# Kernel tuning notes

Measured on AMD Instinct MI355X. Metric: run time of the kernel, lower is better.

## Reference

```python
import jax, jax.numpy as jnp
import numpy as np

H = 16
D_MODEL = 1024
D_K = D_MODEL // H
NEG = -1e9


def setup_inputs() -> dict:
    key = jax.random.key(0)
    ks = jax.random.split(key, 12)
    B, S, D = 2, 2048, D_MODEL
    scale = 1.0 / np.sqrt(D)
    inp = {
        "query": jax.random.normal(ks[0], (B, S, D), jnp.float32),
        "key": jax.random.normal(ks[1], (B, S, D), jnp.float32),
        "value": jax.random.normal(ks[2], (B, S, D), jnp.float32),
        "mask": jax.random.randint(ks[3], (B, S, S), 0, 2, jnp.int32),
        # four Linear(d_model, d_model) layers: q, k, v, out projections
        "Wq": jax.random.normal(ks[4], (D, D), jnp.float32) * scale,
        "bq": jnp.zeros((D,), jnp.float32),
        "Wk": jax.random.normal(ks[5], (D, D), jnp.float32) * scale,
        "bk": jnp.zeros((D,), jnp.float32),
        "Wv": jax.random.normal(ks[6], (D, D), jnp.float32) * scale,
        "bv": jnp.zeros((D,), jnp.float32),
        "Wo": jax.random.normal(ks[7], (D, D), jnp.float32) * scale,
        "bo": jnp.zeros((D,), jnp.float32),
    }
    return inp


def reference(query, key, value, mask, Wq, bq, Wk, bk, Wv, bv, Wo, bo):
    B, S, D = query.shape
    # QKV projections, then split into heads: [B, H, S, D_K]
    def proj(x, W, b):
        return (x @ W + b).reshape(B, S, H, D_K).transpose(0, 2, 1, 3)

    q = proj(query, Wq, bq)
    k = proj(key, Wk, bk)
    v = proj(value, Wv, bv)

    # scaled dot-product attention; scale by sqrt(d_k) (query.size(-1) after split)
    scores = jnp.einsum("bhqd,bhkd->bhqk", q, k) / np.sqrt(D_K)
    scores = jnp.where(mask[:, None, :, :] == 0, NEG, scores)
    p = jax.nn.softmax(scores, axis=-1)  # dropout is identity in eval mode
    x = jnp.einsum("bhqk,bhkd->bhqd", p, v)

    # merge heads and apply output projection
    x = x.transpose(0, 2, 1, 3).reshape(B, S, H * D_K)
    return x @ Wo + bo
```

## Files before the change

### kernel.cpp

```cpp
#include <hip/hip_runtime.h>

typedef _Float16 f16;
typedef __attribute__((ext_vector_type(2))) _Float16 f16x2;
typedef __attribute__((ext_vector_type(4))) _Float16 f16x4;
typedef __attribute__((ext_vector_type(8))) _Float16 f16x8;
typedef __attribute__((ext_vector_type(4))) float f32x4;

#define MFMA16(A_, B_, C_) __builtin_amdgcn_mfma_f32_16x16x32_f16(A_, B_, C_, 0, 0, 0)
#define EXP2(x) __builtin_amdgcn_exp2f(x)

#define NHEAD 16
#define SEQ 2048
#define DM 1024
#define DK 64
#define NBATCH 2
#define M_TOT (NBATCH * SEQ)

#define GLDS(gp, lp)                                                                     \
    __builtin_amdgcn_global_load_lds((const __attribute__((address_space(1))) void*)(gp), \
                                     (__attribute__((address_space(3))) void*)(lp), 16, 0, 0)

__global__ void pack_mask_k(const int* __restrict__ mask, unsigned long long* __restrict__ mp, int nwords) {
    int lane = threadIdx.x & 63;
    int gw = (blockIdx.x * blockDim.x + threadIdx.x) >> 6;
    int nw = (gridDim.x * blockDim.x) >> 6;
    for (int w = gw; w < nwords; w += nw) {
        int v = mask[(size_t)w * 64 + lane];
        unsigned long long bits = __ballot(v != 0);
        if (lane == 0) mp[w] = bits;
    }
}

__global__ __launch_bounds__(256) void cvt_x_k(const float* __restrict__ xq, const float* __restrict__ xk,
                                               const float* __restrict__ xv, f16* __restrict__ oq,
                                               f16* __restrict__ ok, f16* __restrict__ ov) {
    const float* src = blockIdx.z == 0 ? xq : (blockIdx.z == 1 ? xk : xv);
    f16* dst = blockIdx.z == 0 ? oq : (blockIdx.z == 1 ? ok : ov);
    size_t i = ((size_t)blockIdx.x * 256 + threadIdx.x) * 8;
    float4 a = *(const float4*)&src[i];
    float4 b = *(const float4*)&src[i + 4];
    f16x8 h;
    h[0] = (f16)a.x; h[1] = (f16)a.y; h[2] = (f16)a.z; h[3] = (f16)a.w;
    h[4] = (f16)b.x; h[5] = (f16)b.y; h[6] = (f16)b.z; h[7] = (f16)b.w;
    *(f16x8*)&dst[i] = h;
}

__global__ __launch_bounds__(256) void wt_k(const float* __restrict__ Wq, const float* __restrict__ Wk,
                                            const float* __restrict__ Wv, const float* __restrict__ Wo,
                                            f16* __restrict__ Wt) {
    __shared__ float T[64][65];
    const int z = blockIdx.z;
    const float* W = z == 0 ? Wq : (z == 1 ? Wk : (z == 2 ? Wv : Wo));
    f16* out = Wt + (size_t)z * DM * DM;
    const int k0 = blockIdx.y * 64, n0 = blockIdx.x * 64;
    const int r = threadIdx.x >> 2, q = threadIdx.x & 3;
    const float4* s = (const float4*)&W[(size_t)(k0 + r) * DM + n0 + q * 16];
    float4 v0 = s[0], v1 = s[1], v2 = s[2], v3 = s[3];
    T[r][q * 16 + 0] = v0.x; T[r][q * 16 + 1] = v0.y; T[r][q * 16 + 2] = v0.z; T[r][q * 16 + 3] = v0.w;
    T[r][q * 16 + 4] = v1.x; T[r][q * 16 + 5] = v1.y; T[r][q * 16 + 6] = v1.z; T[r][q * 16 + 7] = v1.w;
    T[r][q * 16 + 8] = v2.x; T[r][q * 16 + 9] = v2.y; T[r][q * 16 + 10] = v2.z; T[r][q * 16 + 11] = v2.w;
    T[r][q * 16 + 12] = v3.x; T[r][q * 16 + 13] = v3.y; T[r][q * 16 + 14] = v3.z; T[r][q * 16 + 15] = v3.w;
    __syncthreads();
    f16x8 h0, h1;
#pragma unroll
    for (int j = 0; j < 8; ++j) {
        h0[j] = (f16)T[q * 16 + j][r];
        h1[j] = (f16)T[q * 16 + 8 + j][r];
    }
    *(f16x8*)&out[(size_t)(n0 + r) * DM + k0 + q * 16] = h0;
    *(f16x8*)&out[(size_t)(n0 + r) * DM + k0 + q * 16 + 8] = h1;
}

__global__ __launch_bounds__(256) void vt_k(const f16* __restrict__ Vh, f16* __restrict__ VhT) {
    __shared__ f16 T[64][72];
    const int bh = blockIdx.y;
    const int s0 = blockIdx.x * 64;
    const f16* src = Vh + (size_t)bh * SEQ * DK;
    f16* dst = VhT + (size_t)bh * DK * SEQ;
    const int r = threadIdx.x >> 2, q = threadIdx.x & 3;
    f16x8 a = *(const f16x8*)&src[(size_t)(s0 + r) * DK + q * 16];
    f16x8 b = *(const f16x8*)&src[(size_t)(s0 + r) * DK + q * 16 + 8];
    *(f16x8*)&T[r][q * 16] = a;
    *(f16x8*)&T[r][q * 16 + 8] = b;
    __syncthreads();
    f16x8 o0, o1;
#pragma unroll
    for (int j = 0; j < 8; ++j) {
        o0[j] = T[q * 16 + j][r];
        o1[j] = T[q * 16 + 8 + j][r];
    }
    *(f16x8*)&dst[(size_t)r * SEQ + s0 + q * 16] = o0;
    *(f16x8*)&dst[(size_t)r * SEQ + s0 + q * 16 + 8] = o1;
}

__device__ __forceinline__ void gemm_core(const f16* __restrict__ A, const f16* __restrict__ Bt,
                                          int m0, int n0, f16* Al, f16* Bl, f32x4 acc[4][4], int tid) {
    const int lane = tid & 63;
    const int wv = tid >> 6;
    const int wr = wv >> 1, wc = wv & 1;
    const int g = lane >> 4, c = lane & 15;

    for (int k0 = 0; k0 < DM; k0 += 64) {
#pragma unroll
        for (int j = 0; j < 4; ++j) {
            int chunk = j * 256 + tid;
            int row = chunk >> 3, cc = chunk & 7;
            int ccs = cc ^ (row & 7);
            GLDS(&A[(size_t)(m0 + row) * DM + k0 + ccs * 8], &Al[chunk * 8]);
        }
#pragma unroll
        for (int j = 0; j < 4; ++j) {
            int chunk = j * 256 + tid;
            int row = chunk >> 3, cc = chunk & 7;
            int ccs = cc ^ (row & 7);
            GLDS(&Bt[(size_t)(n0 + row) * DM + k0 + ccs * 8], &Bl[chunk * 8]);
        }
        __syncthreads();
#pragma unroll
        for (int ks = 0; ks < 2; ++ks) {
            f16x8 af[4], bf[4];
#pragma unroll
            for (int mi = 0; mi < 4; ++mi) {
                int row = wr * 64 + mi * 16 + c;
                af[mi] = *(const f16x8*)&Al[row * 64 + ((ks * 4 + g) ^ (row & 7)) * 8];
            }
#pragma unroll
            for (int ni = 0; ni < 4; ++ni) {
                int row = wc * 64 + ni * 16 + c;
                bf[ni] = *(const f16x8*)&Bl[row * 64 + ((ks * 4 + g) ^ (row & 7)) * 8];
            }
#pragma unroll
            for (int mi = 0; mi < 4; ++mi)
#pragma unroll
                for (int ni = 0; ni < 4; ++ni)
                    acc[mi][ni] = MFMA16(af[mi], bf[ni], acc[mi][ni]);
        }
        __syncthreads();
    }
}

__global__ __launch_bounds__(256) void gemm_qkv2_k(
    const f16* __restrict__ Xq, const f16* __restrict__ Xk, const f16* __restrict__ Xv,
    const f16* __restrict__ Wt, const float* __restrict__ bq, const float* __restrict__ bk,
    const float* __restrict__ bv, f16* __restrict__ Qh, f16* __restrict__ Kh, f16* __restrict__ Vh) {
    __shared__ f16 Al[128 * 64];
    __shared__ f16 Bl[128 * 64];
    const int which = blockIdx.z;
    const f16* A = which == 0 ? Xq : (which == 1 ? Xk : Xv);
    const f16* Bt = Wt + (size_t)which * DM * DM;
    const float* bias = which == 0 ? bq : (which == 1 ? bk : bv);
    f16* OUT = which == 0 ? Qh : (which == 1 ? Kh : Vh);

    const int tid = threadIdx.x, lane = tid & 63, wv = tid >> 6;
    const int wr = wv >> 1, wc = wv & 1, g = lane >> 4, c = lane & 15;
    const int m0 = blockIdx.y * 128, n0 = blockIdx.x * 128;

    f32x4 acc[4][4] = {};
    gemm_core(A, Bt, m0, n0, Al, Bl, acc, tid);

#pragma unroll
    for (int ni = 0; ni < 4; ++ni) {
        int n = n0 + wc * 64 + ni * 16 + c;
        float bias_n = bias[n];
        int hh = n >> 6, d = n & 63;
#pragma unroll
        for (int mi = 0; mi < 4; ++mi) {
            int mbase = m0 + wr * 64 + mi * 16 + g * 4;
#pragma unroll
            for (int r = 0; r < 4; ++r) {
                int m = mbase + r;
                int bb = m >> 11, s = m & (SEQ - 1);
                OUT[(((size_t)(bb * NHEAD + hh)) * SEQ + s) * DK + d] = (f16)(acc[mi][ni][r] + bias_n);
            }
        }
    }
}

__global__ __launch_bounds__(256) void gemm_out2_k(
    const f16* __restrict__ Xo, const f16* __restrict__ Wto, const float* __restrict__ bo,
    float* __restrict__ OUT) {
    __shared__ f16 Al[128 * 64];
    __shared__ f16 Bl[128 * 64];
    const int tid = threadIdx.x, lane = tid & 63, wv = tid >> 6;
    const int wr = wv >> 1, wc = wv & 1, g = lane >> 4, c = lane & 15;
    const int m0 = blockIdx.y * 128, n0 = blockIdx.x * 128;

    f32x4 acc[4][4] = {};
    gemm_core(Xo, Wto, m0, n0, Al, Bl, acc, tid);

#pragma unroll
    for (int ni = 0; ni < 4; ++ni) {
        int n = n0 + wc * 64 + ni * 16 + c;
        float bias_n = bo[n];
#pragma unroll
        for (int mi = 0; mi < 4; ++mi) {
            int mbase = m0 + wr * 64 + mi * 16 + g * 4;
#pragma unroll
            for (int r = 0; r < 4; ++r) {
                int m = mbase + r;
                OUT[(size_t)m * DM + n] = acc[mi][ni][r] + bias_n;
            }
        }
    }
}

#define QBLK 128
#define NHALF 2
#define KTH (SEQ / 64 / NHALF)
#define CSC 0.18033688011112042f

__global__ __launch_bounds__(512) void attn_k(
    const f16* __restrict__ Qh, const f16* __restrict__ Kh, const f16* __restrict__ VhT,
    const unsigned long long* __restrict__ mp, f16* __restrict__ O0, f16* __restrict__ O1,
    float2* __restrict__ ml) {
    __shared__ f16 Kl[2][4096];
    __shared__ f16 Vl[2][4096];
    __shared__ f16 Plds[8][16 * 72];

    const int tid = threadIdx.x, lane = tid & 63, wv = tid >> 6;
    const int g = lane >> 4, c = lane & 15;
    const int qt = blockIdx.x, hh = blockIdx.y;
    const int b = blockIdx.z >> 1, half = blockIdx.z & 1;
    const size_t headoff = ((size_t)(b * NHEAD + hh)) * SEQ * DK;
    const f16* Qb = Qh + headoff;
    const f16* Kb = Kh + headoff + (size_t)half * (SEQ / NHALF) * DK;
    const f16* VbT = VhT + headoff + (size_t)half * (SEQ / NHALF);

    const int srow = tid >> 3, scc = (tid & 7) ^ (srow & 7);

#define STAGE_ATTN(jj, pp)                                                      \
    do {                                                                        \
        GLDS(&Kb[(size_t)((jj)*64 + srow) * DK + scc * 8], &Kl[pp][tid * 8]);   \
        GLDS(&VbT[(size_t)srow * SEQ + (jj)*64 + scc * 8], &Vl[pp][tid * 8]);   \
    } while (0)

    const int qrow = qt * QBLK + wv * 16 + c;
    f16x8 bq0 = *(const f16x8*)&Qb[(size_t)qrow * DK + g * 8];
    f16x8 bq1 = *(const f16x8*)&Qb[(size_t)qrow * DK + 32 + g * 8];
    bq0 *= (f16)CSC;
    bq1 *= (f16)CSC;

    f32x4 acc[4] = {};
    float l_run = 0.f;

    const unsigned long long* mrow = mp + ((size_t)b * SEQ + qrow) * (SEQ / 64) + half * KTH;
    unsigned long long wq_cur = mrow[0];

    STAGE_ATTN(0, 0);
    int p = 0;
    for (int j = 0; j < KTH; ++j) {
        __syncthreads();
        if (j + 1 < KTH) STAGE_ATTN(j + 1, p ^ 1);
        unsigned long long wq_nxt = (j + 1 < KTH) ? mrow[j + 1] : 0ull;

        f32x4 sc[4];
        __builtin_amdgcn_s_setprio(1);
#pragma unroll
        for (int nk = 0; nk < 4; ++nk) {
            int row = nk * 16 + c;
            f16x8 k0 = *(const f16x8*)&Kl[p][row * 64 + ((g ^ (row & 7)) * 8)];
            f16x8 k1 = *(const f16x8*)&Kl[p][row * 64 + (((4 + g) ^ (row & 7)) * 8)];
            f32x4 z = {};
            z = MFMA16(k0, bq0, z);
            z = MFMA16(k1, bq1, z);
            sc[nk] = z;
        }
        __builtin_amdgcn_s_setprio(0);

        unsigned long long wq = wq_cur >> (g * 4);
        float ps = 0.f;
#pragma unroll
        for (int nk = 0; nk < 4; ++nk) {
            unsigned int nib = (unsigned int)(wq >> (nk * 16)) & 0xFu;
#pragma unroll
            for (int r = 0; r < 4; ++r) {
                float pp = EXP2(sc[nk][r]);
                pp = (nib & (1u << r)) ? pp : 0.f;
                sc[nk][r] = pp;
                ps += pp;
            }
        }
        ps += __shfl_xor(ps, 16);
        ps += __shfl_xor(ps, 32);
        l_run += ps;

#pragma unroll
        for (int nk = 0; nk < 4; ++nk)
#pragma unroll
            for (int r2 = 0; r2 < 2; ++r2) {
                f16x2 pw = {(f16)sc[nk][r2 * 2], (f16)sc[nk][r2 * 2 + 1]};
                *(f16x2*)&Plds[wv][c * 72 + nk * 16 + g * 4 + r2 * 2] = pw;
            }
        f16x8 pb0 = *(const f16x8*)&Plds[wv][c * 72 + g * 8];
        f16x8 pb1 = *(const f16x8*)&Plds[wv][c * 72 + 32 + g * 8];

        __builtin_amdgcn_s_setprio(1);
#pragma unroll
        for (int nd = 0; nd < 4; ++nd) {
            int row = nd * 16 + c;
            f16x8 v0 = *(const f16x8*)&Vl[p][row * 64 + ((g ^ (row & 7)) * 8)];
            f16x8 v1 = *(const f16x8*)&Vl[p][row * 64 + (((4 + g) ^ (row & 7)) * 8)];
            acc[nd] = MFMA16(v0, pb0, acc[nd]);
            acc[nd] = MFMA16(v1, pb1, acc[nd]);
        }
        __builtin_amdgcn_s_setprio(0);

        wq_cur = wq_nxt;
        p ^= 1;
    }

    f16* Opart = half ? O1 : O0;
    {
        float inv = l_run > 0.f ? 1.0f / l_run : 0.f;
        size_t hrow = headoff / DK + qrow;
#pragma unroll
        for (int nd = 0; nd < 4; ++nd) {
            f16x4 o;
#pragma unroll
            for (int r = 0; r < 4; ++r) o[r] = (f16)(acc[nd][r] * inv);
            *(f16x4*)&Opart[hrow * DK + nd * 16 + g * 4] = o;
        }
        if (g == 0) ml[(size_t)half * (M_TOT * NHEAD) + hrow] = make_float2(0.f, l_run);
    }
#undef STAGE_ATTN
}

__global__ __launch_bounds__(256) void combine_k(const f16* __restrict__ O0, const f16* __restrict__ O1,
                                                 const float2* __restrict__ ml, f16* __restrict__ Xo) {
    const int row = blockIdx.x * 32 + (threadIdx.x >> 3);
    const int d0 = (threadIdx.x & 7) * 8;
    const int b = row >> 15, hh = (row >> 11) & 15, q = row & (SEQ - 1);
    float2 a = ml[row];
    float2 bb = ml[(M_TOT * NHEAD) + row];
    float m = fmaxf(a.x, bb.x);
    float w0 = a.y * EXP2(a.x - m);
    float w1 = bb.y * EXP2(bb.x - m);
    float inv = 1.0f / (w0 + w1);
    float a0 = w0 * inv, a1 = w1 * inv;
    f16x8 o0 = *(const f16x8*)&O0[(size_t)row * DK + d0];
    f16x8 o1 = *(const f16x8*)&O1[(size_t)row * DK + d0];
    f16x8 o;
#pragma unroll
    for (int i = 0; i < 8; ++i) o[i] = (f16)(a0 * (float)o0[i] + a1 * (float)o1[i]);
    *(f16x8*)&Xo[((size_t)(b * SEQ + q)) * DM + hh * DK + d0] = o;
}

extern "C" void kernel_launch(void* const* d_in, const int* in_sizes, int n_in,
                              void* d_out, int out_size, void* d_ws, size_t ws_size,
                              hipStream_t stream) {
    const float* query = (const float*)d_in[0];
    const float* key_ = (const float*)d_in[1];
    const float* value = (const float*)d_in[2];
    const int* mask = (const int*)d_in[3];
    const float* Wq = (const float*)d_in[4];
    const float* bq = (const float*)d_in[5];
    const float* Wk = (const float*)d_in[6];
    const float* bk = (const float*)d_in[7];
    const float* Wv = (const float*)d_in[8];
    const float* bv = (const float*)d_in[9];
    const float* Wo = (const float*)d_in[10];
    const float* bo = (const float*)d_in[11];
    float* out = (float*)d_out;

    char* ws = (char*)d_ws;
    const size_t headsz = (size_t)NBATCH * NHEAD * SEQ * DK * sizeof(f16);
    unsigned long long* mp = (unsigned long long*)(ws);
    f16* Qh = (f16*)(ws + (1 << 20));
    f16* Kh = (f16*)(ws + (1 << 20) + headsz);
    f16* Vh = (f16*)(ws + (1 << 20) + 2 * headsz);
    f16* Xhq = (f16*)(ws + (1 << 20) + 3 * headsz);
    f16* Xhk = (f16*)(ws + (1 << 20) + 4 * headsz);
    f16* Xhv = (f16*)(ws + (1 << 20) + 5 * headsz);
    f16* Wt = (f16*)(ws + (1 << 20) + 6 * headsz);
    float2* ml = (float2*)(ws + (1 << 20) + 7 * headsz);
    f16* VhT = Xhq;
    f16* Xo = Xhq;

    int nwords = NBATCH * SEQ * (SEQ / 64);
    hipLaunchKernelGGL(pack_mask_k, dim3(512), dim3(256), 0, stream, mask, mp, nwords);
    hipLaunchKernelGGL(cvt_x_k, dim3(M_TOT * DM / (8 * 256), 1, 3), dim3(256), 0, stream,
                       query, key_, value, Xhq, Xhk, Xhv);
    hipLaunchKernelGGL(wt_k, dim3(DM / 64, DM / 64, 4), dim3(256), 0, stream, Wq, Wk, Wv, Wo, Wt);
    hipLaunchKernelGGL(gemm_qkv2_k, dim3(DM / 128, M_TOT / 128, 3), dim3(256), 0, stream,
                       Xhq, Xhk, Xhv, Wt, bq, bk, bv, Qh, Kh, Vh);
    hipLaunchKernelGGL(vt_k, dim3(SEQ / 64, NBATCH * NHEAD), dim3(256), 0, stream, Vh, VhT);
    hipLaunchKernelGGL(attn_k, dim3(SEQ / QBLK, NHEAD, NBATCH * NHALF), dim3(512), 0, stream,
                       Qh, Kh, VhT, mp, Xhk, Xhv, ml);
    hipLaunchKernelGGL(combine_k, dim3(M_TOT * NHEAD / 32), dim3(256), 0, stream, Xhk, Xhv, ml, Xo);
    hipLaunchKernelGGL(gemm_out2_k, dim3(DM / 128, M_TOT / 128), dim3(256), 0, stream,
                       Xo, Wt + (size_t)3 * DM * DM, bo, out);
}
```

Baseline: 179.4 us.

## Merge prep kernels, write V transposed from GEMM, fold softmax scale into Wq

Folds the mask packing, input conversion and weight transpose into one prep kernel, which removes two launches. The QKV GEMM epilogue now writes V straight into the transposed layout, so the separate transpose kernel goes away. The softmax scale is folded into Wq and bq at prep time, so the per-block Q multiply in attention is dropped. Also changed: the row-sum shuffle reduction moves out of the loop to run once at the end, and the P staging stride is padded to cut LDS bank conflicts. Risks are the transposed V stores, which are scattered 8-byte writes, and an extra fp16 rounding step on the scaled weights.

After: 170.6 us. 5.0% less time.

```diff
diff --git a/kernel.cpp b/kernel.cpp
--- a/kernel.cpp
+++ b/kernel.cpp
@@ -15,82 +15,65 @@
 #define DK 64
 #define NBATCH 2
 #define M_TOT (NBATCH * SEQ)
+#define CSC 0.18033688011112042f
 
 #define GLDS(gp, lp)                                                                     \
     __builtin_amdgcn_global_load_lds((const __attribute__((address_space(1))) void*)(gp), \
                                      (__attribute__((address_space(3))) void*)(lp), 16, 0, 0)
 
-__global__ void pack_mask_k(const int* __restrict__ mask, unsigned long long* __restrict__ mp, int nwords) {
-    int lane = threadIdx.x & 63;
-    int gw = (blockIdx.x * blockDim.x + threadIdx.x) >> 6;
-    int nw = (gridDim.x * blockDim.x) >> 6;
-    for (int w = gw; w < nwords; w += nw) {
-        int v = mask[(size_t)w * 64 + lane];
-        unsigned long long bits = __ballot(v != 0);
-        if (lane == 0) mp[w] = bits;
-    }
-}
-
-__global__ __launch_bounds__(256) void cvt_x_k(const float* __restrict__ xq, const float* __restrict__ xk,
-                                               const float* __restrict__ xv, f16* __restrict__ oq,
-                                               f16* __restrict__ ok, f16* __restrict__ ov) {
-    const float* src = blockIdx.z == 0 ? xq : (blockIdx.z == 1 ? xk : xv);
-    f16* dst = blockIdx.z == 0 ? oq : (blockIdx.z == 1 ? ok : ov);
-    size_t i = ((size_t)blockIdx.x * 256 + threadIdx.x) * 8;
-    float4 a = *(const float4*)&src[i];
-    float4 b = *(const float4*)&src[i + 4];
-    f16x8 h;
-    h[0] = (f16)a.x; h[1] = (f16)a.y; h[2] = (f16)a.z; h[3] = (f16)a.w;
-    h[4] = (f16)b.x; h[5] = (f16)b.y; h[6] = (f16)b.z; h[7] = (f16)b.w;
-    *(f16x8*)&dst[i] = h;
-}
-
-__global__ __launch_bounds__(256) void wt_k(const float* __restrict__ Wq, const float* __restrict__ Wk,
-                                            const float* __restrict__ Wv, const float* __restrict__ Wo,
-                                            f16* __restrict__ Wt) {
+__global__ __launch_bounds__(256) void prep_k(
+    const int* __restrict__ mask, unsigned long long* __restrict__ mp,
+    const float* __restrict__ xq, const float* __restrict__ xk, const float* __restrict__ xv,
+    f16* __restrict__ oq, f16* __restrict__ ok, f16* __restrict__ ov,
+    const float* __restrict__ Wq, const float* __restrict__ Wk,
+    const float* __restrict__ Wv, const float* __restrict__ Wo, f16* __restrict__ Wt) {
     __shared__ float T[64][65];
-    const int z = blockIdx.z;
-    const float* W = z == 0 ? Wq : (z == 1 ? Wk : (z == 2 ? Wv : Wo));
-    f16* out = Wt + (size_t)z * DM * DM;
-    const int k0 = blockIdx.y * 64, n0 = blockIdx.x * 64;
-    const int r = threadIdx.x >> 2, q = threadIdx.x & 3;
-    const float4* s = (const float4*)&W[(size_t)(k0 + r) * DM + n0 + q * 16];
-    float4 v0 = s[0], v1 = s[1], v2 = s[2], v3 = s[3];
-    T[r][q * 16 + 0] = v0.x; T[r][q * 16 + 1] = v0.y; T[r][q * 16 + 2] = v0.z; T[r][q * 16 + 3] = v0.w;
-    T[r][q * 16 + 4] = v1.x; T[r][q * 16 + 5] = v1.y; T[r][q * 16 + 6] = v1.z; T[r][q * 16 + 7] = v1.w;
-    T[r][q * 16 + 8] = v2.x; T[r][q * 16 + 9] = v2.y; T[r][q * 16 + 10] = v2.z; T[r][q * 16 + 11] = v2.w;
-    T[r][q * 16 + 12] = v3.x; T[r][q * 16 + 13] = v3.y; T[r][q * 16 + 14] = v3.z; T[r][q * 16 + 15] = v3.w;
-    __syncthreads();
-    f16x8 h0, h1;
-#pragma unroll
-    for (int j = 0; j < 8; ++j) {
-        h0[j] = (f16)T[q * 16 + j][r];
-        h1[j] = (f16)T[q * 16 + 8 + j][r];
-    }
-    *(f16x8*)&out[(size_t)(n0 + r) * DM + k0 + q * 16] = h0;
-    *(f16x8*)&out[(size_t)(n0 + r) * DM + k0 + q * 16 + 8] = h1;
-}
-
-__global__ __launch_bounds__(256) void vt_k(const f16* __restrict__ Vh, f16* __restrict__ VhT) {
-    __shared__ f16 T[64][72];
-    const int bh = blockIdx.y;
-    const int s0 = blockIdx.x * 64;
-    const f16* src = Vh + (size_t)bh * SEQ * DK;
-    f16* dst = VhT + (size_t)bh * DK * SEQ;
-    const int r = threadIdx.x >> 2, q = threadIdx.x & 3;
-    f16x8 a = *(const f16x8*)&src[(size_t)(s0 + r) * DK + q * 16];
-    f16x8 b = *(const f16x8*)&src[(size_t)(s0 + r) * DK + q * 16 + 8];
-    *(f16x8*)&T[r][q * 16] = a;
-    *(f16x8*)&T[r][q * 16 + 8] = b;
-    __syncthreads();
-    f16x8 o0, o1;
-#pragma unroll
-    for (int j = 0; j < 8; ++j) {
-        o0[j] = T[q * 16 + j][r];
-        o1[j] = T[q * 16 + 8 + j][r];
-    }
-    *(f16x8*)&dst[(size_t)r * SEQ + s0 + q * 16] = o0;
-    *(f16x8*)&dst[(size_t)r * SEQ + s0 + q * 16 + 8] = o1;
+    const int z = blockIdx.z, bx = blockIdx.x, tid = threadIdx.x;
+    if (z < 3) {
+        const float* src = z == 0 ? xq : (z == 1 ? xk : xv);
+        f16* dst = z == 0 ? oq : (z == 1 ? ok : ov);
+        size_t i = ((size_t)bx * 256 + tid) * 8;
+        float4 a = *(const float4*)&src[i];
+        float4 b = *(const float4*)&src[i + 4];
+        f16x8 h;
+        h[0] = (f16)a.x; h[1] = (f16)a.y; h[2] = (f16)a.z; h[3] = (f16)a.w;
+        h[4] = (f16)b.x; h[5] = (f16)b.y; h[6] = (f16)b.z; h[7] = (f16)b.w;
+        *(f16x8*)&dst[i] = h;
+    } else if (z == 3) {
+        if (bx >= 1024) return;
+        const int zz = bx >> 8, t = bx & 255;
+        const float* W = zz == 0 ? Wq : (zz == 1 ? Wk : (zz == 2 ? Wv : Wo));
+        const float wsc = zz == 0 ? CSC : 1.0f;
+        f16* out = Wt + (size_t)zz * DM * DM;
+        const int k0 = (t >> 4) * 64, n0 = (t & 15) * 64;
+        const int r = tid >> 2, q = tid & 3;
+        const float4* s = (const float4*)&W[(size_t)(k0 + r) * DM + n0 + q * 16];
+        float4 v0 = s[0], v1 = s[1], v2 = s[2], v3 = s[3];
+        T[r][q * 16 + 0] = v0.x; T[r][q * 16 + 1] = v0.y; T[r][q * 16 + 2] = v0.z; T[r][q * 16 + 3] = v0.w;
+        T[r][q * 16 + 4] = v1.x; T[r][q * 16 + 5] = v1.y; T[r][q * 16 + 6] = v1.z; T[r][q * 16 + 7] = v1.w;
+        T[r][q * 16 + 8] = v2.x; T[r][q * 16 + 9] = v2.y; T[r][q * 16 + 10] = v2.z; T[r][q * 16 + 11] = v2.w;
+        T[r][q * 16 + 12] = v3.x; T[r][q * 16 + 13] = v3.y; T[r][q * 16 + 14] = v3.z; T[r][q * 16 + 15] = v3.w;
+        __syncthreads();
+        f16x8 h0, h1;
+#pragma unroll
+        for (int j = 0; j < 8; ++j) {
+            h0[j] = (f16)(T[q * 16 + j][r] * wsc);
+            h1[j] = (f16)(T[q * 16 + 8 + j][r] * wsc);
+        }
+        *(f16x8*)&out[(size_t)(n0 + r) * DM + k0 + q * 16] = h0;
+        *(f16x8*)&out[(size_t)(n0 + r) * DM + k0 + q * 16 + 8] = h1;
+    } else {
+        if (bx >= 512) return;
+        int lane = tid & 63;
+        int gw = (bx * 256 + tid) >> 6;
+        const int nw = (512 * 256) >> 6;
+        const int nwords = NBATCH * SEQ * (SEQ / 64);
+        for (int w = gw; w < nwords; w += nw) {
+            int v = mask[(size_t)w * 64 + lane];
+            unsigned long long bits = __ballot(v != 0);
+            if (lane == 0) mp[w] = bits;
+        }
+    }
 }
 
 __device__ __forceinline__ void gemm_core(const f16* __restrict__ A, const f16* __restrict__ Bt,
@@ -142,14 +125,13 @@
 __global__ __launch_bounds__(256) void gemm_qkv2_k(
     const f16* __restrict__ Xq, const f16* __restrict__ Xk, const f16* __restrict__ Xv,
     const f16* __restrict__ Wt, const float* __restrict__ bq, const float* __restrict__ bk,
-    const float* __restrict__ bv, f16* __restrict__ Qh, f16* __restrict__ Kh, f16* __restrict__ Vh) {
+    const float* __restrict__ bv, f16* __restrict__ Qh, f16* __restrict__ Kh, f16* __restrict__ VhT) {
     __shared__ f16 Al[128 * 64];
     __shared__ f16 Bl[128 * 64];
     const int which = blockIdx.z;
     const f16* A = which == 0 ? Xq : (which == 1 ? Xk : Xv);
     const f16* Bt = Wt + (size_t)which * DM * DM;
     const float* bias = which == 0 ? bq : (which == 1 ? bk : bv);
-    f16* OUT = which == 0 ? Qh : (which == 1 ? Kh : Vh);
 
     const int tid = threadIdx.x, lane = tid & 63, wv = tid >> 6;
     const int wr = wv >> 1, wc = wv & 1, g = lane >> 4, c = lane & 15;
@@ -158,19 +140,39 @@
     f32x4 acc[4][4] = {};
     gemm_core(A, Bt, m0, n0, Al, Bl, acc, tid);
 
-#pragma unroll
-    for (int ni = 0; ni < 4; ++ni) {
-        int n = n0 + wc * 64 + ni * 16 + c;
-        float bias_n = bias[n];
-        int hh = n >> 6, d = n & 63;
-#pragma unroll
-        for (int mi = 0; mi < 4; ++mi) {
-            int mbase = m0 + wr * 64 + mi * 16 + g * 4;
-#pragma unroll
-            for (int r = 0; r < 4; ++r) {
-                int m = mbase + r;
-                int bb = m >> 11, s = m & (SEQ - 1);
-                OUT[(((size_t)(bb * NHEAD + hh)) * SEQ + s) * DK + d] = (f16)(acc[mi][ni][r] + bias_n);
+    const float bsc = which == 0 ? CSC : 1.0f;
+    if (which == 2) {
+#pragma unroll
+        for (int ni = 0; ni < 4; ++ni) {
+            int n = n0 + wc * 64 + ni * 16 + c;
+            float bias_n = bias[n];
+            int hh = n >> 6, d = n & 63;
+#pragma unroll
+            for (int mi = 0; mi < 4; ++mi) {
+                int mbase = m0 + wr * 64 + mi * 16 + g * 4;
+                int bb = mbase >> 11, s = mbase & (SEQ - 1);
+                f16x4 o;
+#pragma unroll
+                for (int r = 0; r < 4; ++r) o[r] = (f16)(acc[mi][ni][r] + bias_n);
+                *(f16x4*)&VhT[(((size_t)(bb * NHEAD + hh)) * DK + d) * SEQ + s] = o;
+            }
+        }
+    } else {
+        f16* OUT = which == 0 ? Qh : Kh;
+#pragma unroll
+        for (int ni = 0; ni < 4; ++ni) {
+            int n = n0 + wc * 64 + ni * 16 + c;
+            float bias_n = bias[n] * bsc;
+            int hh = n >> 6, d = n & 63;
+#pragma unroll
+            for (int mi = 0; mi < 4; ++mi) {
+                int mbase = m0 + wr * 64 + mi * 16 + g * 4;
+#pragma unroll
+                for (int r = 0; r < 4; ++r) {
+                    int m = mbase + r;
+                    int bb = m >> 11, s = m & (SEQ - 1);
+                    OUT[(((size_t)(bb * NHEAD + hh)) * SEQ + s) * DK + d] = (f16)(acc[mi][ni][r] + bias_n);
+                }
             }
         }
     }
@@ -207,7 +209,7 @@
 #define QBLK 128
 #define NHALF 2
 #define KTH (SEQ / 64 / NHALF)
-#define CSC 0.18033688011112042f
+#define PSTR 76
 
 __global__ __launch_bounds__(512) void attn_k(
     const f16* __restrict__ Qh, const f16* __restrict__ Kh, const f16* __restrict__ VhT,
@@ -215,7 +217,7 @@
     float2* __restrict__ ml) {
     __shared__ f16 Kl[2][4096];
     __shared__ f16 Vl[2][4096];
-    __shared__ f16 Plds[8][16 * 72];
+    __shared__ f16 Plds[8][16 * PSTR];
 
     const int tid = threadIdx.x, lane = tid & 63, wv = tid >> 6;
     const int g = lane >> 4, c = lane & 15;
@@ -237,8 +239,6 @@
     const int qrow = qt * QBLK + wv * 16 + c;
     f16x8 bq0 = *(const f16x8*)&Qb[(size_t)qrow * DK + g * 8];
     f16x8 bq1 = *(const f16x8*)&Qb[(size_t)qrow * DK + 32 + g * 8];
-    bq0 *= (f16)CSC;
-    bq1 *= (f16)CSC;
 
     f32x4 acc[4] = {};
     float l_run = 0.f;
@@ -280,8 +280,6 @@
                 ps += pp;
             }
         }
-        ps += __shfl_xor(ps, 16);
-        ps += __shfl_xor(ps, 32);
         l_run += ps;
 
 #pragma unroll
@@ -289,10 +287,10 @@
 #pragma unroll
             for (int r2 = 0; r2 < 2; ++r2) {
                 f16x2 pw = {(f16)sc[nk][r2 * 2], (f16)sc[nk][r2 * 2 + 1]};
-                *(f16x2*)&Plds[wv][c * 72 + nk * 16 + g * 4 + r2 * 2] = pw;
-            }
-        f16x8 pb0 = *(const f16x8*)&Plds[wv][c * 72 + g * 8];
-        f16x8 pb1 = *(const f16x8*)&Plds[wv][c * 72 + 32 + g * 8];
+                *(f16x2*)&Plds[wv][c * PSTR + nk * 16 + g * 4 + r2 * 2] = pw;
+            }
+        f16x8 pb0 = *(const f16x8*)&Plds[wv][c * PSTR + g * 8];
+        f16x8 pb1 = *(const f16x8*)&Plds[wv][c * PSTR + 32 + g * 8];
 
         __builtin_amdgcn_s_setprio(1);
 #pragma unroll
@@ -308,6 +306,9 @@
         wq_cur = wq_nxt;
         p ^= 1;
     }
+
+    l_run += __shfl_xor(l_run, 16);
+    l_run += __shfl_xor(l_run, 32);
 
     f16* Opart = half ? O1 : O0;
     {
@@ -367,23 +368,18 @@
     unsigned long long* mp = (unsigned long long*)(ws);
     f16* Qh = (f16*)(ws + (1 << 20));
     f16* Kh = (f16*)(ws + (1 << 20) + headsz);
-    f16* Vh = (f16*)(ws + (1 << 20) + 2 * headsz);
+    f16* VhT = (f16*)(ws + (1 << 20) + 2 * headsz);
     f16* Xhq = (f16*)(ws + (1 << 20) + 3 * headsz);
     f16* Xhk = (f16*)(ws + (1 << 20) + 4 * headsz);
     f16* Xhv = (f16*)(ws + (1 << 20) + 5 * headsz);
     f16* Wt = (f16*)(ws + (1 << 20) + 6 * headsz);
     float2* ml = (float2*)(ws + (1 << 20) + 7 * headsz);
-    f16* VhT = Xhq;
     f16* Xo = Xhq;
 
-    int nwords = NBATCH * SEQ * (SEQ / 64);
-    hipLaunchKernelGGL(pack_mask_k, dim3(512), dim3(256), 0, stream, mask, mp, nwords);
-    hipLaunchKernelGGL(cvt_x_k, dim3(M_TOT * DM / (8 * 256), 1, 3), dim3(256), 0, stream,
-                       query, key_, value, Xhq, Xhk, Xhv);
-    hipLaunchKernelGGL(wt_k, dim3(DM / 64, DM / 64, 4), dim3(256), 0, stream, Wq, Wk, Wv, Wo, Wt);
+    hipLaunchKernelGGL(prep_k, dim3(M_TOT * DM / (8 * 256), 1, 5), dim3(256), 0, stream,
+                       mask, mp, query, key_, value, Xhq, Xhk, Xhv, Wq, Wk, Wv, Wo, Wt);
     hipLaunchKernelGGL(gemm_qkv2_k, dim3(DM / 128, M_TOT / 128, 3), dim3(256), 0, stream,
-                       Xhq, Xhk, Xhv, Wt, bq, bk, bv, Qh, Kh, Vh);
-    hipLaunchKernelGGL(vt_k, dim3(SEQ / 64, NBATCH * NHEAD), dim3(256), 0, stream, Vh, VhT);
+                       Xhq, Xhk, Xhv, Wt, bq, bk, bv, Qh, Kh, VhT);
     hipLaunchKernelGGL(attn_k, dim3(SEQ / QBLK, NHEAD, NBATCH * NHALF), dim3(512), 0, stream,
                        Qh, Kh, VhT, mp, Xhk, Xhv, ml);
     hipLaunchKernelGGL(combine_k, dim3(M_TOT * NHEAD / 32), dim3(256), 0, stream, Xhk, Xhv, ml, Xo);
```
